# Optimization experiments

Hardware: AMD Instinct MI355X
Metric: run time of the kernel (lower is better)

The kernel has to match this reference:

```python
import jax, jax.numpy as jnp
import numpy as np

IN_FEATURES = 4096
LOCAL_FEATURES = 128
KERNEL_SIZE = 64
STRIDE = 32
FOLD_NUM = (IN_FEATURES - KERNEL_SIZE) // STRIDE + 1  # 127
BATCH = 4096


def setup_inputs() -> dict:
    key = jax.random.key(0)
    kx, kw, kb = jax.random.split(key, 3)
    x = jax.random.normal(kx, (BATCH, IN_FEATURES), dtype=jnp.float32)
    # Per-window linear weights: torch Linear weight is [out, in] = [local_features, kernel_size]
    bound = 1.0 / np.sqrt(KERNEL_SIZE)
    W = jax.random.uniform(kw, (FOLD_NUM, LOCAL_FEATURES, KERNEL_SIZE),
                           dtype=jnp.float32, minval=-bound, maxval=bound)
    b = jax.random.uniform(kb, (FOLD_NUM, LOCAL_FEATURES),
                           dtype=jnp.float32, minval=-bound, maxval=bound)
    return {"x": x, "W": W, "b": b}


def reference(x, W, b) -> jnp.ndarray:
    # Unfold: windows[f, k] = x[:, f*stride + k] -> [B, FOLD_NUM, KERNEL_SIZE]
    idx = jnp.arange(FOLD_NUM)[:, None] * STRIDE + jnp.arange(KERNEL_SIZE)[None, :]
    windows = x[:, idx]  # [B, F, K]
    # Batched per-window linear: out[b, f, l] = sum_k windows[b,f,k] * W[f,l,k] + b[f,l]
    out = jnp.einsum('bfk,flk->bfl', windows, W) + b[None, :, :]
    # torch.cat along dim 1 over fold index == reshape [B, F*L]
    return out.reshape(x.shape[0], FOLD_NUM * LOCAL_FEATURES)
```

## Files before the change

### kernel.cpp

```cpp
#include <hip/hip_runtime.h>
#include <hip/hip_bf16.h>

#define IN_F 4096
#define LOCAL_F 128
#define KSZ 64
#define STRIDE_ 32
#define FOLDS 127
#define BATCH_ 4096
#define OUT_F (FOLDS * LOCAL_F)
#define WN (FOLDS * LOCAL_F * KSZ)

#define ROWS 16
#define FPB 8
#define LDSW (FPB * LOCAL_F + 4)

typedef __attribute__((ext_vector_type(8))) short bf16x8;
typedef __attribute__((ext_vector_type(8))) unsigned short u16x8;
typedef __attribute__((ext_vector_type(4))) float f32x4;

__device__ __forceinline__ unsigned short f2bf(float f) {
    unsigned u = __builtin_bit_cast(unsigned, f);
    u += 0x7fffu + ((u >> 16) & 1u);
    return (unsigned short)(u >> 16);
}

__global__ __launch_bounds__(256)
void wprep_kernel(const float* __restrict__ W, unsigned short* __restrict__ Wbf) {
    int i = (blockIdx.x * 256 + threadIdx.x) * 8;
    if (i >= WN) return;
    float4 a = *reinterpret_cast<const float4*>(W + i);
    float4 c = *reinterpret_cast<const float4*>(W + i + 4);
    u16x8 s;
    s[0] = f2bf(a.x); s[1] = f2bf(a.y); s[2] = f2bf(a.z); s[3] = f2bf(a.w);
    s[4] = f2bf(c.x); s[5] = f2bf(c.y); s[6] = f2bf(c.z); s[7] = f2bf(c.w);
    *reinterpret_cast<u16x8*>(Wbf + i) = s;
}

__global__ __launch_bounds__(256, 2)
void ll_main(const float* __restrict__ x,
             const unsigned short* __restrict__ Wbf,
             const float* __restrict__ b,
             float* __restrict__ out) {
    __shared__ float os[ROWS][LDSW];

    const int fqb = blockIdx.x;
    const int rg  = blockIdx.y;
    const int row0 = rg * ROWS;

    const int wave = threadIdx.x >> 6;
    const int lane = threadIdx.x & 63;
    const int l16 = lane & 15;
    const int g   = lane >> 4;

    #pragma unroll
    for (int p = 0; p < 2; ++p) {
        const int fl = wave * 2 + p;
        const int f  = fqb * FPB + fl;
        if (f < FOLDS) {
            const float* xp = x + (size_t)(row0 + l16) * IN_F + f * STRIDE_ + g * 8;
            float4 xa0 = *reinterpret_cast<const float4*>(xp);
            float4 xa1 = *reinterpret_cast<const float4*>(xp + 4);
            float4 xb0 = *reinterpret_cast<const float4*>(xp + 32);
            float4 xb1 = *reinterpret_cast<const float4*>(xp + 36);

            const unsigned short* Wf = Wbf + (size_t)f * (LOCAL_F * KSZ) + l16 * KSZ + g * 8;
            bf16x8 wf[2][8];
            #pragma unroll
            for (int nt = 0; nt < 8; ++nt) {
                wf[0][nt] = *reinterpret_cast<const bf16x8*>(Wf + nt * 16 * KSZ);
                wf[1][nt] = *reinterpret_cast<const bf16x8*>(Wf + nt * 16 * KSZ + 32);
            }

            bf16x8 af0, af1;
            af0[0] = (short)f2bf(xa0.x); af0[1] = (short)f2bf(xa0.y);
            af0[2] = (short)f2bf(xa0.z); af0[3] = (short)f2bf(xa0.w);
            af0[4] = (short)f2bf(xa1.x); af0[5] = (short)f2bf(xa1.y);
            af0[6] = (short)f2bf(xa1.z); af0[7] = (short)f2bf(xa1.w);
            af1[0] = (short)f2bf(xb0.x); af1[1] = (short)f2bf(xb0.y);
            af1[2] = (short)f2bf(xb0.z); af1[3] = (short)f2bf(xb0.w);
            af1[4] = (short)f2bf(xb1.x); af1[5] = (short)f2bf(xb1.y);
            af1[6] = (short)f2bf(xb1.z); af1[7] = (short)f2bf(xb1.w);

            f32x4 acc[8];
            #pragma unroll
            for (int nt = 0; nt < 8; ++nt) acc[nt] = (f32x4){0.f, 0.f, 0.f, 0.f};
            #pragma unroll
            for (int nt = 0; nt < 8; ++nt)
                acc[nt] = __builtin_amdgcn_mfma_f32_16x16x32_bf16(wf[0][nt], af0, acc[nt], 0, 0, 0);
            #pragma unroll
            for (int nt = 0; nt < 8; ++nt)
                acc[nt] = __builtin_amdgcn_mfma_f32_16x16x32_bf16(wf[1][nt], af1, acc[nt], 0, 0, 0);

            #pragma unroll
            for (int nt = 0; nt < 8; ++nt) {
                f32x4 bv = *reinterpret_cast<const f32x4*>(b + (size_t)f * LOCAL_F + nt * 16 + 4 * g);
                f32x4 v = acc[nt] + bv;
                *reinterpret_cast<f32x4*>(&os[l16][fl * LOCAL_F + nt * 16 + 4 * g]) = v;
            }
        }
    }
    __syncthreads();

    const int t = threadIdx.x;
    const int colbase = fqb * (FPB * LOCAL_F);
    const int col = colbase + 4 * t;
    #pragma unroll
    for (int r = 0; r < ROWS; ++r) {
        if (col < OUT_F) {
            f32x4 v = *reinterpret_cast<const f32x4*>(&os[r][4 * t]);
            *reinterpret_cast<f32x4*>(out + (size_t)(row0 + r) * OUT_F + col) = v;
        }
    }
}

extern "C" void kernel_launch(void* const* d_in, const int* in_sizes, int n_in,
                              void* d_out, int out_size, void* d_ws, size_t ws_size,
                              hipStream_t stream) {
    const float* x = (const float*)d_in[0];
    const float* W = (const float*)d_in[1];
    const float* b = (const float*)d_in[2];
    float* out = (float*)d_out;
    unsigned short* Wbf = (unsigned short*)d_ws;

    wprep_kernel<<<(WN / 8 + 255) / 256, 256, 0, stream>>>(W, Wbf);
    dim3 grid(16, BATCH_ / ROWS);
    ll_main<<<grid, 256, 0, stream>>>(x, Wbf, b, out);
}
```

Measured before the change: 127.2 us.

## Use persistent XCD-swizzled blocks looping over tiles with nontemporal x loads

Replaces the 16x256 grid with 512 blocks that each process 8 consecutive tiles. The block index is remapped so each XCD handles a contiguous range of row/fold tiles. This aims to improve L2 locality of weights and input rows across chiplets, and to cut block launch overhead. Input x is loaded with nontemporal hints to avoid cache pollution. In exchange, fewer resident blocks and an extra barrier per tile may reduce latency hiding.

```diff
diff --git a/kernel.cpp b/kernel.cpp
--- a/kernel.cpp
+++ b/kernel.cpp
@@ -43,72 +43,81 @@
              float* __restrict__ out) {
     __shared__ float os[ROWS][LDSW];
 
-    const int fqb = blockIdx.x;
-    const int rg  = blockIdx.y;
-    const int row0 = rg * ROWS;
+    const int l = blockIdx.x;
+    const int j = l & 7;
+    const int k = l >> 3;
 
     const int wave = threadIdx.x >> 6;
     const int lane = threadIdx.x & 63;
     const int l16 = lane & 15;
     const int g   = lane >> 4;
 
-    #pragma unroll
-    for (int p = 0; p < 2; ++p) {
-        const int fl = wave * 2 + p;
-        const int f  = fqb * FPB + fl;
-        if (f < FOLDS) {
-            const float* xp = x + (size_t)(row0 + l16) * IN_F + f * STRIDE_ + g * 8;
-            float4 xa0 = *reinterpret_cast<const float4*>(xp);
-            float4 xa1 = *reinterpret_cast<const float4*>(xp + 4);
-            float4 xb0 = *reinterpret_cast<const float4*>(xp + 32);
-            float4 xb1 = *reinterpret_cast<const float4*>(xp + 36);
+    for (int i = 0; i < 8; ++i) {
+        const int v   = (j * 64 + k) * 8 + i;
+        const int rg  = v >> 4;
+        const int fqb = v & 15;
+        const int row0 = rg * ROWS;
 
-            const unsigned short* Wf = Wbf + (size_t)f * (LOCAL_F * KSZ) + l16 * KSZ + g * 8;
-            bf16x8 wf[2][8];
-            #pragma unroll
-            for (int nt = 0; nt < 8; ++nt) {
-                wf[0][nt] = *reinterpret_cast<const bf16x8*>(Wf + nt * 16 * KSZ);
-                wf[1][nt] = *reinterpret_cast<const bf16x8*>(Wf + nt * 16 * KSZ + 32);
-            }
+        if (i != 0) __syncthreads();
 
-            bf16x8 af0, af1;
-            af0[0] = (short)f2bf(xa0.x); af0[1] = (short)f2bf(xa0.y);
-            af0[2] = (short)f2bf(xa0.z); af0[3] = (short)f2bf(xa0.w);
-            af0[4] = (short)f2bf(xa1.x); af0[5] = (short)f2bf(xa1.y);
-            af0[6] = (short)f2bf(xa1.z); af0[7] = (short)f2bf(xa1.w);
-            af1[0] = (short)f2bf(xb0.x); af1[1] = (short)f2bf(xb0.y);
-            af1[2] = (short)f2bf(xb0.z); af1[3] = (short)f2bf(xb0.w);
-            af1[4] = (short)f2bf(xb1.x); af1[5] = (short)f2bf(xb1.y);
-            af1[6] = (short)f2bf(xb1.z); af1[7] = (short)f2bf(xb1.w);
+        #pragma unroll
+        for (int p = 0; p < 2; ++p) {
+            const int fl = wave * 2 + p;
+            const int f  = fqb * FPB + fl;
+            if (f < FOLDS) {
+                const float* xp = x + (size_t)(row0 + l16) * IN_F + f * STRIDE_ + g * 8;
+                f32x4 xa0 = __builtin_nontemporal_load(reinterpret_cast<const f32x4*>(xp));
+                f32x4 xa1 = __builtin_nontemporal_load(reinterpret_cast<const f32x4*>(xp + 4));
+                f32x4 xb0 = __builtin_nontemporal_load(reinterpret_cast<const f32x4*>(xp + 32));
+                f32x4 xb1 = __builtin_nontemporal_load(reinterpret_cast<const f32x4*>(xp + 36));
 
-            f32x4 acc[8];
-            #pragma unroll
-            for (int nt = 0; nt < 8; ++nt) acc[nt] = (f32x4){0.f, 0.f, 0.f, 0.f};
-            #pragma unroll
-            for (int nt = 0; nt < 8; ++nt)
-                acc[nt] = __builtin_amdgcn_mfma_f32_16x16x32_bf16(wf[0][nt], af0, acc[nt], 0, 0, 0);
-            #pragma unroll
-            for (int nt = 0; nt < 8; ++nt)
-                acc[nt] = __builtin_amdgcn_mfma_f32_16x16x32_bf16(wf[1][nt], af1, acc[nt], 0, 0, 0);
+                const unsigned short* Wf = Wbf + (size_t)f * (LOCAL_F * KSZ) + l16 * KSZ + g * 8;
+                bf16x8 wf[2][8];
+                #pragma unroll
+                for (int nt = 0; nt < 8; ++nt) {
+                    wf[0][nt] = *reinterpret_cast<const bf16x8*>(Wf + nt * 16 * KSZ);
+                    wf[1][nt] = *reinterpret_cast<const bf16x8*>(Wf + nt * 16 * KSZ + 32);
+                }
 
-            #pragma unroll
-            for (int nt = 0; nt < 8; ++nt) {
-                f32x4 bv = *reinterpret_cast<const f32x4*>(b + (size_t)f * LOCAL_F + nt * 16 + 4 * g);
-                f32x4 v = acc[nt] + bv;
-                *reinterpret_cast<f32x4*>(&os[l16][fl * LOCAL_F + nt * 16 + 4 * g]) = v;
+                bf16x8 af0, af1;
+                af0[0] = (short)f2bf(xa0[0]); af0[1] = (short)f2bf(xa0[1]);
+                af0[2] = (short)f2bf(xa0[2]); af0[3] = (short)f2bf(xa0[3]);
+                af0[4] = (short)f2bf(xa1[0]); af0[5] = (short)f2bf(xa1[1]);
+                af0[6] = (short)f2bf(xa1[2]); af0[7] = (short)f2bf(xa1[3]);
+                af1[0] = (short)f2bf(xb0[0]); af1[1] = (short)f2bf(xb0[1]);
+                af1[2] = (short)f2bf(xb0[2]); af1[3] = (short)f2bf(xb0[3]);
+                af1[4] = (short)f2bf(xb1[0]); af1[5] = (short)f2bf(xb1[1]);
+                af1[6] = (short)f2bf(xb1[2]); af1[7] = (short)f2bf(xb1[3]);
+
+                f32x4 acc[8];
+                #pragma unroll
+                for (int nt = 0; nt < 8; ++nt) acc[nt] = (f32x4){0.f, 0.f, 0.f, 0.f};
+                #pragma unroll
+                for (int nt = 0; nt < 8; ++nt)
+                    acc[nt] = __builtin_amdgcn_mfma_f32_16x16x32_bf16(wf[0][nt], af0, acc[nt], 0, 0, 0);
+                #pragma unroll
+                for (int nt = 0; nt < 8; ++nt)
+                    acc[nt] = __builtin_amdgcn_mfma_f32_16x16x32_bf16(wf[1][nt], af1, acc[nt], 0, 0, 0);
+
+                #pragma unroll
+                for (int nt = 0; nt < 8; ++nt) {
+                    f32x4 bv = *reinterpret_cast<const f32x4*>(b + (size_t)f * LOCAL_F + nt * 16 + 4 * g);
+                    f32x4 vv = acc[nt] + bv;
+                    *reinterpret_cast<f32x4*>(&os[l16][fl * LOCAL_F + nt * 16 + 4 * g]) = vv;
+                }
             }
         }
-    }
-    __syncthreads();
+        __syncthreads();
 
-    const int t = threadIdx.x;
-    const int colbase = fqb * (FPB * LOCAL_F);
-    const int col = colbase + 4 * t;
-    #pragma unroll
-    for (int r = 0; r < ROWS; ++r) {
-        if (col < OUT_F) {
-            f32x4 v = *reinterpret_cast<const f32x4*>(&os[r][4 * t]);
-            *reinterpret_cast<f32x4*>(out + (size_t)(row0 + r) * OUT_F + col) = v;
+        const int t = threadIdx.x;
+        const int colbase = fqb * (FPB * LOCAL_F);
+        const int col = colbase + 4 * t;
+        #pragma unroll
+        for (int r = 0; r < ROWS; ++r) {
+            if (col < OUT_F) {
+                f32x4 vv = *reinterpret_cast<const f32x4*>(&os[r][4 * t]);
+                *reinterpret_cast<f32x4*>(out + (size_t)(row0 + r) * OUT_F + col) = vv;
+            }
         }
     }
 }
@@ -123,6 +132,5 @@
     unsigned short* Wbf = (unsigned short*)d_ws;
 
     wprep_kernel<<<(WN / 8 + 255) / 256, 256, 0, stream>>>(W, Wbf);
-    dim3 grid(16, BATCH_ / ROWS);
-    ll_main<<<grid, 256, 0, stream>>>(x, Wbf, b, out);
+    ll_main<<<dim3(512), 256, 0, stream>>>(x, Wbf, b, out);
 }
```

New measurement: 141.4 us. +11.2%, slower.
